# Optimization experiments

Hardware: AMD Instinct MI355X
Metric: run time of the kernel (lower is better)

## Reference

```python
import jax, jax.numpy as jnp
import numpy as np

NUM_HEAD = 16
EMBED_DIM = 1024
HEAD_DIM = EMBED_DIM // NUM_HEAD
QK_DIM = EMBED_DIM  # qk_dim defaults to embed_dim


def setup_inputs() -> dict:
    key = jax.random.key(0)
    k1, k2, k3 = jax.random.split(key, 3)
    x = jax.random.normal(k1, (4, 2048, EMBED_DIM), dtype=jnp.float32)
    # xavier_uniform-like init scale
    lim_qkv = float(np.sqrt(6.0 / (EMBED_DIM + 3 * EMBED_DIM)))
    lim_out = float(np.sqrt(6.0 / (EMBED_DIM + EMBED_DIM)))
    W_QKV = jax.random.uniform(k2, (EMBED_DIM, 3 * EMBED_DIM), jnp.float32, -lim_qkv, lim_qkv)
    W_Out = jax.random.uniform(k3, (EMBED_DIM, EMBED_DIM), jnp.float32, -lim_out, lim_out)
    return {"x": x, "W_QKV": W_QKV, "W_Out": W_Out}


def reference(x, W_QKV, W_Out):
    bsz, slen, _ = x.shape
    # [b,s,3E] -> [b,s,H,hd,3] -> [b,H,s,hd,3]  (interleaved qkv layout, as in torch source)
    qkv = (x @ W_QKV).reshape(bsz, slen, NUM_HEAD, HEAD_DIM, 3).transpose(0, 2, 1, 3, 4)
    q, k, v = qkv[..., 0], qkv[..., 1], qkv[..., 2]
    # NOTE: module scales by sqrt(qk_dim) (full dim), not sqrt(head_dim)
    scores = jnp.einsum("bhqd,bhkd->bhqk", q, k) / np.sqrt(QK_DIM).astype(np.float32)
    attn = jax.nn.softmax(scores, axis=-1)  # dropout p=0.0 -> identity
    out = jnp.einsum("bhqk,bhkd->bhqd", attn, v)  # [b,H,s,hd]
    out = out.transpose(0, 2, 1, 3).reshape(bsz, slen, EMBED_DIM)
    return out @ W_Out
```

## Files before the change

kernel.cpp:

```cpp
#include <hip/hip_runtime.h>
#include <stdint.h>

typedef __bf16 bf16x8 __attribute__((ext_vector_type(8)));
typedef __bf16 bf16x4_t __attribute__((ext_vector_type(4)));
typedef float f32x4 __attribute__((ext_vector_type(4)));
typedef unsigned short u16x8 __attribute__((ext_vector_type(8)));
typedef unsigned short u16x4 __attribute__((ext_vector_type(4)));
typedef short s16x4 __attribute__((ext_vector_type(4)));
typedef unsigned int u32x2 __attribute__((ext_vector_type(2)));

#if __has_builtin(__builtin_amdgcn_mfma_f32_16x16x16bf16_1k)
#define MFMA16X16X16(a, b, c) __builtin_amdgcn_mfma_f32_16x16x16bf16_1k((a), (b), (c), 0, 0, 0)
#elif __has_builtin(__builtin_amdgcn_mfma_f32_16x16x16_bf16)
#define MFMA16X16X16(a, b, c)                                                             \
    __builtin_amdgcn_mfma_f32_16x16x16_bf16(__builtin_bit_cast(bf16x4_t, (a)),            \
                                            __builtin_bit_cast(bf16x4_t, (b)), (c), 0, 0, 0)
#else
static __device__ __forceinline__ f32x4 MFMA16X16X16(s16x4, s16x4, f32x4 c) { return c; }
#endif

#if __has_builtin(__builtin_amdgcn_exp2f)
#define EXP2(x) __builtin_amdgcn_exp2f(x)
#else
#define EXP2(x) exp2f(x)
#endif

__device__ __forceinline__ unsigned short f2bf(float f) {
    unsigned int u = __float_as_uint(f);
    u += 0x7fffu + ((u >> 16) & 1u);
    return (unsigned short)(u >> 16);
}

__device__ __forceinline__ unsigned int pack2_bf16(float f0, float f1) {
    unsigned int u0 = __float_as_uint(f0) + 0x8000u;
    unsigned int u1 = __float_as_uint(f1) + 0x8000u;
#if __has_builtin(__builtin_amdgcn_perm)
    return __builtin_amdgcn_perm(u1, u0, 0x07060302u);
#else
    return (u0 >> 16) | (u1 & 0xffff0000u);
#endif
}

__device__ __forceinline__ int swz64(int row, int c) {
    return (c & 7) | ((((c >> 3) ^ row) & 7) << 3);
}

__device__ __forceinline__ void glds16(const unsigned short* g, unsigned short* l) {
    __builtin_amdgcn_global_load_lds((const __attribute__((address_space(1))) void*)g,
                                     (__attribute__((address_space(3))) void*)l, 16, 0, 0);
}

__global__ __launch_bounds__(256) void cast_x_kernel(const float* __restrict__ in,
                                                     unsigned short* __restrict__ out) {
    size_t id = (size_t)blockIdx.x * 256 + threadIdx.x;
    int row = (int)(id >> 7);
    int cid = (int)(id & 127);
    const float4* src = (const float4*)(in + id * 8);
    float4 a = src[0], b = src[1];
    u16x8 o;
    o[0] = f2bf(a.x); o[1] = f2bf(a.y); o[2] = f2bf(a.z); o[3] = f2bf(a.w);
    o[4] = f2bf(b.x); o[5] = f2bf(b.y); o[6] = f2bf(b.z); o[7] = f2bf(b.w);
    int group = cid >> 3, ch = cid & 7;
    *(u16x8*)(out + (size_t)row * 1024 + group * 64 + (((ch ^ row) & 7) << 3)) = o;
}

__global__ __launch_bounds__(256) void transpose_cast_kernel(const float* __restrict__ in,
                                                             unsigned short* __restrict__ out,
                                                             int K, int N) {
    __shared__ unsigned short tile[32][33];
    int nb = blockIdx.x * 32, kb = blockIdx.y * 32;
    int tx = threadIdx.x & 31, ty = threadIdx.x >> 5;
    #pragma unroll
    for (int r = ty; r < 32; r += 8)
        tile[r][tx] = f2bf(in[(size_t)(kb + r) * N + nb + tx]);
    __syncthreads();
    #pragma unroll
    for (int r = ty; r < 32; r += 8) {
        int row = nb + r, col = kb + tx;
        out[(size_t)row * K + (col & ~63) + swz64(row, col & 63)] = tile[tx][r];
    }
}

__device__ __forceinline__ void gemm128_mainloop(const unsigned short* __restrict__ A,
                                                 const unsigned short* __restrict__ Bt,
                                                 int K, f32x4 acc[4][4]) {
    __shared__ unsigned short As[128 * 64];
    __shared__ unsigned short Bs[128 * 64];
    const int t = threadIdx.x, lane = t & 63, w = t >> 6;
    const int wm = w & 1, wn = w >> 1;
    const int r16 = lane & 15, quad = lane >> 4;
    const size_t mb = (size_t)blockIdx.y * 128, nb = (size_t)blockIdx.x * 128;

    const f32x4 zf = {0.f, 0.f, 0.f, 0.f};
    #pragma unroll
    for (int i = 0; i < 4; i++)
        #pragma unroll
        for (int j = 0; j < 4; j++) acc[i][j] = zf;

    for (int kt = 0; kt < K; kt += 64) {
        __syncthreads();
        #pragma unroll
        for (int c = 0; c < 4; c++) {
            int r = w * 32 + c * 8 + (lane >> 3);
            int col = (lane & 7) * 8;
            glds16(A + (mb + r) * K + kt + col, &As[(w * 32 + c * 8) * 64]);
            glds16(Bt + (nb + r) * K + kt + col, &Bs[(w * 32 + c * 8) * 64]);
        }
        __syncthreads();
        #pragma unroll
        for (int kkh = 0; kkh < 2; kkh++) {
            int kk = kkh * 32;
            bf16x8 af[4], bf[4];
            #pragma unroll
            for (int i = 0; i < 4; i++) {
                int row = wm * 64 + i * 16 + r16;
                af[i] = *(const bf16x8*)(&As[row * 64 + ((((kk >> 3) + quad) ^ (row & 7)) << 3)]);
            }
            #pragma unroll
            for (int j = 0; j < 4; j++) {
                int row = wn * 64 + j * 16 + r16;
                bf[j] = *(const bf16x8*)(&Bs[row * 64 + ((((kk >> 3) + quad) ^ (row & 7)) << 3)]);
            }
            #pragma unroll
            for (int i = 0; i < 4; i++)
                #pragma unroll
                for (int j = 0; j < 4; j++)
                    acc[i][j] = __builtin_amdgcn_mfma_f32_16x16x32_bf16(af[i], bf[j], acc[i][j], 0, 0, 0);
        }
    }
}

__global__ __launch_bounds__(256) void gemm_qkv_kernel(const unsigned short* __restrict__ A,
                                                       const unsigned short* __restrict__ Bt,
                                                       unsigned short* __restrict__ Qo,
                                                       unsigned short* __restrict__ Ko,
                                                       unsigned short* __restrict__ Vo) {
    f32x4 acc[4][4];
    gemm128_mainloop(A, Bt, 1024, acc);
    const int t = threadIdx.x, lane = t & 63, w = t >> 6;
    const int wm = w & 1, wn = w >> 1;
    const int c16 = lane & 15, quad = lane >> 4;
    const int mb = blockIdx.y * 128, nb = blockIdx.x * 128;
    const float SCALE_Q = 1.4426950408889634f / 32.0f;
    #pragma unroll
    for (int i = 0; i < 4; i++) {
        #pragma unroll
        for (int j = 0; j < 4; j++) {
            #pragma unroll
            for (int r = 0; r < 4; r++) {
                int m = mb + wm * 64 + i * 16 + quad * 4 + r;
                int n = nb + wn * 64 + j * 16 + c16;
                float v = acc[i][j][r];
                int b = m >> 11, s = m & 2047;
                int h = n / 192, rem = n % 192;
                int d = rem / 3, c = rem - 3 * d;
                int bh = b * 16 + h;
                if (c == 0)
                    Qo[((size_t)bh * 2048 + s) * 64 + swz64(s, d)] = f2bf(v * SCALE_Q);
                else if (c == 1)
                    Ko[((size_t)bh * 2048 + s) * 64 + swz64(s, d)] = f2bf(v);
                else
                    Vo[((size_t)bh * 64 + d) * 2048 + (s & ~63) + swz64(d, s & 63)] = f2bf(v);
            }
        }
    }
}

__global__ __launch_bounds__(256) void gemm_out_kernel(const unsigned short* __restrict__ A,
                                                       const unsigned short* __restrict__ Bt,
                                                       float* __restrict__ C) {
    f32x4 acc[4][4];
    gemm128_mainloop(A, Bt, 1024, acc);
    const int t = threadIdx.x, lane = t & 63, w = t >> 6;
    const int wm = w & 1, wn = w >> 1;
    const int c16 = lane & 15, quad = lane >> 4;
    const int mb = blockIdx.y * 128, nb = blockIdx.x * 128;
    #pragma unroll
    for (int i = 0; i < 4; i++)
        #pragma unroll
        for (int j = 0; j < 4; j++)
            #pragma unroll
            for (int r = 0; r < 4; r++) {
                int m = mb + wm * 64 + i * 16 + quad * 4 + r;
                int n = nb + wn * 64 + j * 16 + c16;
                C[(size_t)m * 1024 + n] = acc[i][j][r];
            }
}

__global__ __launch_bounds__(256) void attn_kernel(const unsigned short* __restrict__ Qg,
                                                   const unsigned short* __restrict__ Kg,
                                                   const unsigned short* __restrict__ Vt,
                                                   unsigned short* __restrict__ O) {
    __shared__ unsigned short Ks[2][64 * 64];
    __shared__ unsigned short Vs[2][64 * 64];
    const int t = threadIdx.x, lane = t & 63, w = t >> 6;
    const int c16 = lane & 15, quad = lane >> 4;
    const int bh = blockIdx.y, q0 = blockIdx.x * 128;

    bf16x8 qf[2][2];
    #pragma unroll
    for (int qt = 0; qt < 2; qt++) {
        int row = q0 + w * 32 + qt * 16 + c16;
        #pragma unroll
        for (int kkh = 0; kkh < 2; kkh++) {
            int c = kkh * 32 + quad * 8;
            qf[qt][kkh] = *(const bf16x8*)(Qg + ((size_t)bh * 2048 + row) * 64 + swz64(row, c));
        }
    }

    auto stage = [&](int buf, int k0) {
        #pragma unroll
        for (int c = 0; c < 2; c++) {
            int r = w * 16 + c * 8 + (lane >> 3);
            int col = (lane & 7) * 8;
            glds16(Kg + ((size_t)bh * 2048 + k0 + r) * 64 + col, &Ks[buf][(w * 16 + c * 8) * 64]);
            glds16(Vt + ((size_t)bh * 64 + r) * 2048 + k0 + col, &Vs[buf][(w * 16 + c * 8) * 64]);
        }
    };

    const f32x4 zf = {0.f, 0.f, 0.f, 0.f};
    f32x4 acc_o[2][4];
    float den[2] = {0.f, 0.f};
    #pragma unroll
    for (int qt = 0; qt < 2; qt++)
        #pragma unroll
        for (int dt = 0; dt < 4; dt++) acc_o[qt][dt] = zf;

    stage(0, 0);
    for (int it = 0; it < 32; it++) {
        __syncthreads();
        if (it < 31) stage((it + 1) & 1, (it + 1) * 64);
        const unsigned short* ks = Ks[it & 1];
        const unsigned short* vs = Vs[it & 1];

        f32x4 sacc[4][2];
        #pragma unroll
        for (int kt = 0; kt < 4; kt++)
            #pragma unroll
            for (int qt = 0; qt < 2; qt++) sacc[kt][qt] = zf;
        #pragma unroll
        for (int kkh = 0; kkh < 2; kkh++) {
            bf16x8 kf[4];
            #pragma unroll
            for (int kt = 0; kt < 4; kt++) {
                int row = kt * 16 + c16;
                kf[kt] = *(const bf16x8*)(ks + row * 64 + swz64(row, kkh * 32 + quad * 8));
            }
            #pragma unroll
            for (int kt = 0; kt < 4; kt++)
                #pragma unroll
                for (int qt = 0; qt < 2; qt++)
                    sacc[kt][qt] = __builtin_amdgcn_mfma_f32_16x16x32_bf16(kf[kt], qf[qt][kkh],
                                                                           sacc[kt][qt], 0, 0, 0);
        }

        #pragma unroll
        for (int kt = 0; kt < 4; kt++) {
            s16x4 vf[4];
            #pragma unroll
            for (int dt = 0; dt < 4; dt++) {
                int row = dt * 16 + c16;
                vf[dt] = *(const s16x4*)(vs + row * 64 + swz64(row, kt * 16 + quad * 4));
            }
            #pragma unroll
            for (int qt = 0; qt < 2; qt++) {
                float e0 = EXP2(sacc[kt][qt][0]);
                float e1 = EXP2(sacc[kt][qt][1]);
                float e2 = EXP2(sacc[kt][qt][2]);
                float e3 = EXP2(sacc[kt][qt][3]);
                den[qt] += (e0 + e1) + (e2 + e3);
                u32x2 uu = {pack2_bf16(e0, e1), pack2_bf16(e2, e3)};
                s16x4 pk = __builtin_bit_cast(s16x4, uu);
                #pragma unroll
                for (int dt = 0; dt < 4; dt++)
                    acc_o[qt][dt] = MFMA16X16X16(pk, vf[dt], acc_o[qt][dt]);
            }
        }
    }

    #pragma unroll
    for (int qt = 0; qt < 2; qt++) {
        den[qt] += __shfl_xor(den[qt], 16);
        den[qt] += __shfl_xor(den[qt], 32);
    }

    const int b = bh >> 4, h = bh & 15;
    #pragma unroll
    for (int qt = 0; qt < 2; qt++) {
        #pragma unroll
        for (int r = 0; r < 4; r++) {
            float rd = 1.0f / __shfl(den[qt], quad * 4 + r);
            int srow = q0 + w * 32 + qt * 16 + quad * 4 + r;
            #pragma unroll
            for (int dt = 0; dt < 4; dt++) {
                int col = dt * 16 + c16;
                O[((size_t)b * 2048 + srow) * 1024 + h * 64 + swz64(srow, col)] =
                    f2bf(acc_o[qt][dt][r] * rd);
            }
        }
    }
}

extern "C" void kernel_launch(void* const* d_in, const int* in_sizes, int n_in,
                              void* d_out, int out_size, void* d_ws, size_t ws_size,
                              hipStream_t stream) {
    (void)in_sizes; (void)n_in; (void)out_size; (void)ws_size;
    const float* x = (const float*)d_in[0];
    const float* wqkv = (const float*)d_in[1];
    const float* wout = (const float*)d_in[2];
    float* out = (float*)d_out;

    const size_t SZ_X = 8388608;
    const size_t SZ_WQKV = 3145728;
    const size_t SZ_WOUT = 1048576;

    unsigned short* ws = (unsigned short*)d_ws;
    unsigned short* xb = ws;
    unsigned short* wqkvt = xb + SZ_X;
    unsigned short* woutt = wqkvt + SZ_WQKV;
    unsigned short* Qa = woutt + SZ_WOUT;
    unsigned short* Ka = Qa + SZ_X;
    unsigned short* Va = Ka + SZ_X;
    unsigned short* attn = Va + SZ_X;

    cast_x_kernel<<<4096, 256, 0, stream>>>(x, xb);
    transpose_cast_kernel<<<dim3(96, 32), 256, 0, stream>>>(wqkv, wqkvt, 1024, 3072);
    transpose_cast_kernel<<<dim3(32, 32), 256, 0, stream>>>(wout, woutt, 1024, 1024);
    gemm_qkv_kernel<<<dim3(24, 64), 256, 0, stream>>>(xb, wqkvt, Qa, Ka, Va);
    attn_kernel<<<dim3(16, 64), 256, 0, stream>>>(Qa, Ka, Va, attn);
    gemm_out_kernel<<<dim3(8, 64), 256, 0, stream>>>(attn, woutt, out);
}
```

Baseline: 318.4 us.

## Double-buffer GEMM LDS tiles and pre-permute QKV weight columns by class

The GEMM mainloop now uses two LDS buffers, issuing the global-to-LDS loads for the next K tile before computing on the current one, with a single barrier per iteration. Separately, the QKV weight transpose reorders output columns into Q/K/V-major, head-major order, so each GEMM block writes a single class and head. That replaces the per-element div/mod and three-way branch in the epilogue with uniform, more contiguous stores. The cost is doubled LDS use (64KB per block), which may reduce occupancy.

```diff
diff --git a/kernel.cpp b/kernel.cpp
--- a/kernel.cpp
+++ b/kernel.cpp
@@ -66,7 +66,7 @@
 
 __global__ __launch_bounds__(256) void transpose_cast_kernel(const float* __restrict__ in,
                                                              unsigned short* __restrict__ out,
-                                                             int K, int N) {
+                                                             int K, int N, int permute) {
     __shared__ unsigned short tile[32][33];
     int nb = blockIdx.x * 32, kb = blockIdx.y * 32;
     int tx = threadIdx.x & 31, ty = threadIdx.x >> 5;
@@ -76,7 +76,15 @@
     __syncthreads();
     #pragma unroll
     for (int r = ty; r < 32; r += 8) {
-        int row = nb + r, col = kb + tx;
+        int n_orig = nb + r, col = kb + tx;
+        int row;
+        if (permute) {
+            int h = n_orig / 192, rem = n_orig - h * 192;
+            int d = rem / 3, cc = rem - 3 * d;
+            row = cc * 1024 + h * 64 + d;
+        } else {
+            row = n_orig;
+        }
         out[(size_t)row * K + (col & ~63) + swz64(row, col & 63)] = tile[tx][r];
     }
 }
@@ -84,8 +92,8 @@
 __device__ __forceinline__ void gemm128_mainloop(const unsigned short* __restrict__ A,
                                                  const unsigned short* __restrict__ Bt,
                                                  int K, f32x4 acc[4][4]) {
-    __shared__ unsigned short As[128 * 64];
-    __shared__ unsigned short Bs[128 * 64];
+    __shared__ unsigned short As[2][128 * 64];
+    __shared__ unsigned short Bs[2][128 * 64];
     const int t = threadIdx.x, lane = t & 63, w = t >> 6;
     const int wm = w & 1, wn = w >> 1;
     const int r16 = lane & 15, quad = lane >> 4;
@@ -97,16 +105,23 @@
         #pragma unroll
         for (int j = 0; j < 4; j++) acc[i][j] = zf;
 
-    for (int kt = 0; kt < K; kt += 64) {
-        __syncthreads();
+    auto stage = [&](int buf, int kt) {
         #pragma unroll
         for (int c = 0; c < 4; c++) {
             int r = w * 32 + c * 8 + (lane >> 3);
             int col = (lane & 7) * 8;
-            glds16(A + (mb + r) * K + kt + col, &As[(w * 32 + c * 8) * 64]);
-            glds16(Bt + (nb + r) * K + kt + col, &Bs[(w * 32 + c * 8) * 64]);
-        }
+            glds16(A + (mb + r) * K + kt + col, &As[buf][(w * 32 + c * 8) * 64]);
+            glds16(Bt + (nb + r) * K + kt + col, &Bs[buf][(w * 32 + c * 8) * 64]);
+        }
+    };
+
+    const int nkt = K >> 6;
+    stage(0, 0);
+    for (int it = 0; it < nkt; it++) {
         __syncthreads();
+        if (it + 1 < nkt) stage((it + 1) & 1, (it + 1) << 6);
+        const unsigned short* as = As[it & 1];
+        const unsigned short* bs = Bs[it & 1];
         #pragma unroll
         for (int kkh = 0; kkh < 2; kkh++) {
             int kk = kkh * 32;
@@ -114,12 +129,12 @@
             #pragma unroll
             for (int i = 0; i < 4; i++) {
                 int row = wm * 64 + i * 16 + r16;
-                af[i] = *(const bf16x8*)(&As[row * 64 + ((((kk >> 3) + quad) ^ (row & 7)) << 3)]);
+                af[i] = *(const bf16x8*)(&as[row * 64 + ((((kk >> 3) + quad) ^ (row & 7)) << 3)]);
             }
             #pragma unroll
             for (int j = 0; j < 4; j++) {
                 int row = wn * 64 + j * 16 + r16;
-                bf[j] = *(const bf16x8*)(&Bs[row * 64 + ((((kk >> 3) + quad) ^ (row & 7)) << 3)]);
+                bf[j] = *(const bf16x8*)(&bs[row * 64 + ((((kk >> 3) + quad) ^ (row & 7)) << 3)]);
             }
             #pragma unroll
             for (int i = 0; i < 4; i++)
@@ -141,23 +156,23 @@
     const int wm = w & 1, wn = w >> 1;
     const int c16 = lane & 15, quad = lane >> 4;
     const int mb = blockIdx.y * 128, nb = blockIdx.x * 128;
+    const int cls = nb >> 10;
+    const int hh = ((nb & 1023) >> 6) + wn;
     const float SCALE_Q = 1.4426950408889634f / 32.0f;
     #pragma unroll
     for (int i = 0; i < 4; i++) {
         #pragma unroll
-        for (int j = 0; j < 4; j++) {
-            #pragma unroll
-            for (int r = 0; r < 4; r++) {
-                int m = mb + wm * 64 + i * 16 + quad * 4 + r;
-                int n = nb + wn * 64 + j * 16 + c16;
+        for (int r = 0; r < 4; r++) {
+            int m = mb + wm * 64 + i * 16 + quad * 4 + r;
+            int b = m >> 11, s = m & 2047;
+            int bh = b * 16 + hh;
+            #pragma unroll
+            for (int j = 0; j < 4; j++) {
+                int d = j * 16 + c16;
                 float v = acc[i][j][r];
-                int b = m >> 11, s = m & 2047;
-                int h = n / 192, rem = n % 192;
-                int d = rem / 3, c = rem - 3 * d;
-                int bh = b * 16 + h;
-                if (c == 0)
+                if (cls == 0)
                     Qo[((size_t)bh * 2048 + s) * 64 + swz64(s, d)] = f2bf(v * SCALE_Q);
-                else if (c == 1)
+                else if (cls == 1)
                     Ko[((size_t)bh * 2048 + s) * 64 + swz64(s, d)] = f2bf(v);
                 else
                     Vo[((size_t)bh * 64 + d) * 2048 + (s & ~63) + swz64(d, s & 63)] = f2bf(v);
@@ -324,8 +339,8 @@
     unsigned short* attn = Va + SZ_X;
 
     cast_x_kernel<<<4096, 256, 0, stream>>>(x, xb);
-    transpose_cast_kernel<<<dim3(96, 32), 256, 0, stream>>>(wqkv, wqkvt, 1024, 3072);
-    transpose_cast_kernel<<<dim3(32, 32), 256, 0, stream>>>(wout, woutt, 1024, 1024);
+    transpose_cast_kernel<<<dim3(96, 32), 256, 0, stream>>>(wqkv, wqkvt, 1024, 3072, 1);
+    transpose_cast_kernel<<<dim3(32, 32), 256, 0, stream>>>(wout, woutt, 1024, 1024, 0);
     gemm_qkv_kernel<<<dim3(24, 64), 256, 0, stream>>>(xb, wqkvt, Qa, Ka, Va);
     attn_kernel<<<dim3(16, 64), 256, 0, stream>>>(Qa, Ka, Va, attn);
     gemm_out_kernel<<<dim3(8, 64), 256, 0, stream>>>(attn, woutt, out);
```

Result: faster. 300.0 us (-5.8%).
